# Optimization experiments

Measured on AMD Instinct MI355X. Metric: run time of the kernel, lower is better.

The kernel has to match this reference:

```python
import jax, jax.numpy as jnp
import numpy as np

N = 50000
E = 800000
P = 400000
D_IN = 128
D_HID = 128


def setup_inputs() -> dict:
    key = jax.random.key(0)
    k = jax.random.split(key, 7)
    edge_index = jax.random.randint(k[0], (2, E), 0, N, dtype=jnp.int32)
    edge_pairs = jax.random.randint(k[1], (2, P), 0, N, dtype=jnp.int32)
    emb = jax.random.normal(k[2], (N, D_IN), dtype=jnp.float32)
    W1 = jax.random.normal(k[3], (D_IN, D_HID), dtype=jnp.float32) * (1.0 / np.sqrt(D_IN))
    b1 = jnp.zeros((D_HID,), dtype=jnp.float32)
    W2 = jax.random.normal(k[4], (D_HID, D_HID), dtype=jnp.float32) * (1.0 / np.sqrt(D_HID))
    b2 = jnp.zeros((D_HID,), dtype=jnp.float32)
    return {"edge_index": edge_index, "edge_pairs": edge_pairs, "emb": emb,
            "W1": W1, "b1": b1, "W2": W2, "b2": b2}


def gcn_conv(x, W, b, src, dst):
    """PyG GCNConv: add self-loops, symmetric deg^-1/2 normalization,
    linear transform, scatter-add aggregation into destination nodes."""
    n = x.shape[0]
    loop = jnp.arange(n, dtype=src.dtype)
    s = jnp.concatenate([src, loop])  # [E+N]
    d = jnp.concatenate([dst, loop])
    deg = jax.ops.segment_sum(jnp.ones_like(d, dtype=x.dtype), d, num_segments=n)
    dinv = jnp.where(deg > 0, jax.lax.rsqrt(jnp.maximum(deg, 1e-12)), 0.0)
    norm = dinv[s] * dinv[d]  # [E+N]
    h = x @ W  # [N, out]
    msg = h[s] * norm[:, None]  # gather + scale
    out = jax.ops.segment_sum(msg, d, num_segments=n)  # scatter-add
    return out + b


def reference(edge_index, edge_pairs, emb, W1, b1, W2, b2):
    src, dst = edge_index[0], edge_index[1]
    # encode (eval mode: dropout is identity)
    z = jax.nn.relu(gcn_conv(emb, W1, b1, src, dst))
    z = gcn_conv(z, W2, b2, src, dst)
    # decode: dot product per candidate pair
    return jnp.sum(z[edge_pairs[0]] * z[edge_pairs[1]], axis=1)  # [P]
```

## Files before the change

kernel.cpp:

```cpp
#include <hip/hip_runtime.h>


typedef __attribute__((ext_vector_type(8))) short short8;
typedef __attribute__((ext_vector_type(4))) float floatx4;

#define STAGE_G 128

__device__ __forceinline__ unsigned short f2bf(float f) {
    union { float f; unsigned int u; } v; v.f = f;
    unsigned int u = v.u;
    u += 0x7fffu + ((u >> 16) & 1u);
    return (unsigned short)(u >> 16);
}

__device__ __forceinline__ unsigned int pack2(float a, float b) {
    return (unsigned int)f2bf(a) | ((unsigned int)f2bf(b) << 16);
}

__device__ __forceinline__ float4 cvt4(unsigned int lo, unsigned int hi) {
    float4 f;
    f.x = __uint_as_float(lo << 16);
    f.y = __uint_as_float(lo & 0xffff0000u);
    f.z = __uint_as_float(hi << 16);
    f.w = __uint_as_float(hi & 0xffff0000u);
    return f;
}


__global__ __launch_bounds__(256) void block_hist_kernel(const int* __restrict__ dst,
                                                         int* __restrict__ bhist,
                                                         int E, int NB) {
    __shared__ int bh[1024];
    int t = threadIdx.x, g = blockIdx.x;
    for (int b = t; b < NB; b += 256) bh[b] = 0;
    __syncthreads();
    int chunk = (E + gridDim.x - 1) / gridDim.x;
    int lo = g * chunk, hi = min(lo + chunk, E);
    for (int i = lo + t; i < hi; i += 256) atomicAdd(&bh[dst[i] >> 6], 1);
    __syncthreads();
    for (int b = t; b < NB; b += 256) bhist[g * NB + b] = bh[b];
}

__global__ __launch_bounds__(128) void s1_scan_blocks(int* __restrict__ bhist,
                                                      int* __restrict__ T, int NB) {
    __shared__ int s[2][128];
    int b = blockIdx.x, t = threadIdx.x;
    int v = bhist[t * NB + b];
    int cur = 0;
    s[0][t] = v;
    __syncthreads();
#pragma unroll
    for (int off = 1; off < 128; off <<= 1) {
        int nxt = cur ^ 1;
        int val = s[cur][t];
        if (t >= off) val += s[cur][t - off];
        s[nxt][t] = val;
        __syncthreads();
        cur = nxt;
    }
    int inc = s[cur][t];
    bhist[t * NB + b] = inc - v;
    if (t == 127) T[b] = inc;
}

__global__ __launch_bounds__(256) void s2_scan_buckets(const int* __restrict__ T,
                                                       int* __restrict__ bucket_base, int NB) {
    __shared__ int sums[256];
    int t = threadIdx.x;
    int chunk = (NB + 255) >> 8;
    int lo = t * chunk, hi = min(lo + chunk, NB);
    int s = 0;
    for (int i = lo; i < hi; ++i) s += T[i];
    sums[t] = s;
    __syncthreads();
    if (t == 0) {
        int run = 0;
        for (int i = 0; i < 256; ++i) { int v = sums[i]; sums[i] = run; run += v; }
    }
    __syncthreads();
    int run = sums[t];
    for (int i = lo; i < hi; ++i) { bucket_base[i] = run; run += T[i]; }
    if (lo < NB && hi == NB) bucket_base[NB] = run;
}

__global__ __launch_bounds__(256) void stage_kernel(const int* __restrict__ src,
                                                    const int* __restrict__ dst,
                                                    const int* __restrict__ bhist,
                                                    const int* __restrict__ bucket_base,
                                                    unsigned int* __restrict__ stage,
                                                    int E, int NB) {
    __shared__ int lcur[1024];
    int t = threadIdx.x, g = blockIdx.x;
    for (int b = t; b < NB; b += 256) lcur[b] = bucket_base[b] + bhist[g * NB + b];
    __syncthreads();
    int chunk = (E + gridDim.x - 1) / gridDim.x;
    int lo = g * chunk, hi = min(lo + chunk, E);
    for (int i = lo + t; i < hi; i += 256) {
        int d = dst[i];
        int pos = atomicAdd(&lcur[d >> 6], 1);
        stage[pos] = ((unsigned int)src[i] << 6) | (unsigned int)(d & 63);
    }
}

__global__ __launch_bounds__(256) void scatter_kernel(const unsigned int* __restrict__ stage,
                                                      const int* __restrict__ bucket_base,
                                                      int* __restrict__ row_ptr,
                                                      float* __restrict__ dinv,
                                                      int* __restrict__ srcs_sorted,
                                                      int N) {
    __shared__ int cnt[64];
    __shared__ int lcur[64];
    int b = blockIdx.x, t = threadIdx.x;
    int lo = b << 6;
    int base = bucket_base[b], basen = bucket_base[b + 1];
    if (t < 64) cnt[t] = 0;
    __syncthreads();
    for (int i = base + t; i < basen; i += 256) atomicAdd(&cnt[stage[i] & 63u], 1);
    __syncthreads();
    if (t < 64) {
        int v = cnt[t];
        int inc = v;
#pragma unroll
        for (int off = 1; off < 64; off <<= 1) {
            int x = __shfl_up(inc, off, 64);
            if (t >= off) inc += x;
        }
        int exc = inc - v;
        int node = lo + t;
        if (node < N) {
            row_ptr[node] = base + exc;
            dinv[node] = rsqrtf((float)(v + 1));
            if (node == N - 1) row_ptr[N] = base + exc + v;
        }
        lcur[t] = base + exc;
    }
    __syncthreads();
    for (int i = base + t; i < basen; i += 256) {
        unsigned int rec = stage[i];
        int pos = atomicAdd(&lcur[rec & 63u], 1);
        srcs_sorted[pos] = (int)(rec >> 6);
    }
}

template <bool BF16IN>
__global__ __launch_bounds__(256) void gemm_mfma_kernel(const void* __restrict__ Xv,
                                                        const float* __restrict__ W,
                                                        const float* __restrict__ dinv,
                                                        uint2* __restrict__ H, int N) {
    __shared__ __align__(16) char smem[50176];
    short* WB = (short*)smem;
    short* XL = (short*)(smem + 32768);
    float* Cst = (float*)smem;

    const int tid = threadIdx.x;
    const int w = tid >> 6;
    const int lane = tid & 63;
    const int blk = blockIdx.x;

    {
        const float4* W4 = (const float4*)W;
#pragma unroll
        for (int i = 0; i < 16; ++i) {
            int f = tid + i * 256;
            int k = f >> 5;
            int c4 = f & 31;
            float4 wv = W4[f];
            int kt = k >> 5, q = (k >> 3) & 3, j = k & 7;
            float e[4] = {wv.x, wv.y, wv.z, wv.w};
#pragma unroll
            for (int m = 0; m < 4; ++m) {
                int c = c4 * 4 + m;
                int nt = c >> 4;
                int ln = q * 16 + (c & 15);
                WB[((nt * 4 + kt) * 64 + ln) * 8 + j] = (short)f2bf(e[m]);
            }
        }
    }
    {
#pragma unroll
        for (int i = 0; i < 8; ++i) {
            int f = tid + i * 256;
            int row = f >> 5;
            int c4 = f & 31;
            int gr = min(blk * 64 + row, N - 1);
            uint2 u;
            if constexpr (BF16IN) {
                u = ((const uint2*)Xv)[(size_t)gr * 32 + c4];
            } else {
                float4 xv = ((const float4*)Xv)[(size_t)gr * 32 + c4];
                u.x = pack2(xv.x, xv.y);
                u.y = pack2(xv.z, xv.w);
            }
            *(uint2*)&XL[row * 136 + c4 * 4] = u;
        }
    }
    __syncthreads();

    const int arow = w * 16 + (lane & 15);
    const int koff = (lane >> 4) * 8;
    short8 a[4];
#pragma unroll
    for (int kt = 0; kt < 4; ++kt)
        a[kt] = *(const short8*)&XL[arow * 136 + kt * 32 + koff];

    floatx4 acc[8];
#pragma unroll
    for (int nt = 0; nt < 8; ++nt) acc[nt] = (floatx4){0.f, 0.f, 0.f, 0.f};

#pragma unroll
    for (int kt = 0; kt < 4; ++kt) {
#pragma unroll
        for (int nt = 0; nt < 8; ++nt) {
            short8 b = *(const short8*)&WB[((nt * 4 + kt) * 64 + lane) * 8];
            acc[nt] = __builtin_amdgcn_mfma_f32_16x16x32_bf16(a[kt], b, acc[nt], 0, 0, 0);
        }
    }
    __syncthreads();

    {
        int q = lane >> 4, cn = lane & 15;
#pragma unroll
        for (int nt = 0; nt < 8; ++nt)
#pragma unroll
            for (int r = 0; r < 4; ++r)
                Cst[(w * 16 + q * 4 + r) * 132 + nt * 16 + cn] = acc[nt][r];
    }
    __syncthreads();
    {
#pragma unroll
        for (int i = 0; i < 8; ++i) {
            int f = tid + i * 256;
            int row = f >> 5;
            int c4 = f & 31;
            int gr = blk * 64 + row;
            if (gr < N) {
                float4 v = *(float4*)&Cst[row * 132 + c4 * 4];
                float di = dinv[gr];
                uint2 o;
                o.x = pack2(v.x * di, v.y * di);
                o.y = pack2(v.z * di, v.w * di);
                H[(size_t)gr * 32 + c4] = o;
            }
        }
    }
}

__global__ __launch_bounds__(256) void agg_kernel(const unsigned short* __restrict__ Hp,
                                                  const int* __restrict__ row_ptr,
                                                  const int* __restrict__ srcs,
                                                  const float* __restrict__ dinv,
                                                  const float* __restrict__ bias,
                                                  unsigned short* __restrict__ Z,
                                                  int N, int do_relu) {
    int gw = (int)((blockIdx.x * blockDim.x + threadIdx.x) >> 6);
    int lane = threadIdx.x & 63;
    int q = lane >> 4;
    int hl = lane & 15;
    int n = gw * 4 + q;
    if (n >= N) return;

    const uint4* H4 = (const uint4*)Hp;
    uint4 us = H4[(size_t)n * 16 + hl];
    float4 a0 = cvt4(us.x, us.y);
    float4 a1 = cvt4(us.z, us.w);
    float4 b0 = make_float4(0.f, 0.f, 0.f, 0.f);
    float4 b1 = make_float4(0.f, 0.f, 0.f, 0.f);

    int j = row_ptr[n], end = row_ptr[n + 1];
    for (; j + 7 < end; j += 8) {
        uint4 u0 = H4[(size_t)srcs[j + 0] * 16 + hl];
        uint4 u1 = H4[(size_t)srcs[j + 1] * 16 + hl];
        uint4 u2 = H4[(size_t)srcs[j + 2] * 16 + hl];
        uint4 u3 = H4[(size_t)srcs[j + 3] * 16 + hl];
        uint4 u4 = H4[(size_t)srcs[j + 4] * 16 + hl];
        uint4 u5 = H4[(size_t)srcs[j + 5] * 16 + hl];
        uint4 u6 = H4[(size_t)srcs[j + 6] * 16 + hl];
        uint4 u7 = H4[(size_t)srcs[j + 7] * 16 + hl];
        float4 t;
        t = cvt4(u0.x, u0.y); a0.x += t.x; a0.y += t.y; a0.z += t.z; a0.w += t.w;
        t = cvt4(u0.z, u0.w); a1.x += t.x; a1.y += t.y; a1.z += t.z; a1.w += t.w;
        t = cvt4(u1.x, u1.y); b0.x += t.x; b0.y += t.y; b0.z += t.z; b0.w += t.w;
        t = cvt4(u1.z, u1.w); b1.x += t.x; b1.y += t.y; b1.z += t.z; b1.w += t.w;
        t = cvt4(u2.x, u2.y); a0.x += t.x; a0.y += t.y; a0.z += t.z; a0.w += t.w;
        t = cvt4(u2.z, u2.w); a1.x += t.x; a1.y += t.y; a1.z += t.z; a1.w += t.w;
        t = cvt4(u3.x, u3.y); b0.x += t.x; b0.y += t.y; b0.z += t.z; b0.w += t.w;
        t = cvt4(u3.z, u3.w); b1.x += t.x; b1.y += t.y; b1.z += t.z; b1.w += t.w;
        t = cvt4(u4.x, u4.y); a0.x += t.x; a0.y += t.y; a0.z += t.z; a0.w += t.w;
        t = cvt4(u4.z, u4.w); a1.x += t.x; a1.y += t.y; a1.z += t.z; a1.w += t.w;
        t = cvt4(u5.x, u5.y); b0.x += t.x; b0.y += t.y; b0.z += t.z; b0.w += t.w;
        t = cvt4(u5.z, u5.w); b1.x += t.x; b1.y += t.y; b1.z += t.z; b1.w += t.w;
        t = cvt4(u6.x, u6.y); a0.x += t.x; a0.y += t.y; a0.z += t.z; a0.w += t.w;
        t = cvt4(u6.z, u6.w); a1.x += t.x; a1.y += t.y; a1.z += t.z; a1.w += t.w;
        t = cvt4(u7.x, u7.y); b0.x += t.x; b0.y += t.y; b0.z += t.z; b0.w += t.w;
        t = cvt4(u7.z, u7.w); b1.x += t.x; b1.y += t.y; b1.z += t.z; b1.w += t.w;
    }
    for (; j + 3 < end; j += 4) {
        uint4 u0 = H4[(size_t)srcs[j + 0] * 16 + hl];
        uint4 u1 = H4[(size_t)srcs[j + 1] * 16 + hl];
        uint4 u2 = H4[(size_t)srcs[j + 2] * 16 + hl];
        uint4 u3 = H4[(size_t)srcs[j + 3] * 16 + hl];
        float4 t;
        t = cvt4(u0.x, u0.y); a0.x += t.x; a0.y += t.y; a0.z += t.z; a0.w += t.w;
        t = cvt4(u0.z, u0.w); a1.x += t.x; a1.y += t.y; a1.z += t.z; a1.w += t.w;
        t = cvt4(u1.x, u1.y); b0.x += t.x; b0.y += t.y; b0.z += t.z; b0.w += t.w;
        t = cvt4(u1.z, u1.w); b1.x += t.x; b1.y += t.y; b1.z += t.z; b1.w += t.w;
        t = cvt4(u2.x, u2.y); a0.x += t.x; a0.y += t.y; a0.z += t.z; a0.w += t.w;
        t = cvt4(u2.z, u2.w); a1.x += t.x; a1.y += t.y; a1.z += t.z; a1.w += t.w;
        t = cvt4(u3.x, u3.y); b0.x += t.x; b0.y += t.y; b0.z += t.z; b0.w += t.w;
        t = cvt4(u3.z, u3.w); b1.x += t.x; b1.y += t.y; b1.z += t.z; b1.w += t.w;
    }
    for (; j < end; ++j) {
        uint4 u = H4[(size_t)srcs[j] * 16 + hl];
        float4 t;
        t = cvt4(u.x, u.y); a0.x += t.x; a0.y += t.y; a0.z += t.z; a0.w += t.w;
        t = cvt4(u.z, u.w); a1.x += t.x; a1.y += t.y; a1.z += t.z; a1.w += t.w;
    }
    a0.x += b0.x; a0.y += b0.y; a0.z += b0.z; a0.w += b0.w;
    a1.x += b1.x; a1.y += b1.y; a1.z += b1.z; a1.w += b1.w;

    float di = dinv[n];
    float4 bv0 = ((const float4*)bias)[2 * hl];
    float4 bv1 = ((const float4*)bias)[2 * hl + 1];
    float o0 = di * a0.x + bv0.x, o1 = di * a0.y + bv0.y;
    float o2 = di * a0.z + bv0.z, o3 = di * a0.w + bv0.w;
    float o4 = di * a1.x + bv1.x, o5 = di * a1.y + bv1.y;
    float o6 = di * a1.z + bv1.z, o7 = di * a1.w + bv1.w;
    if (do_relu) {
        o0 = fmaxf(o0, 0.f); o1 = fmaxf(o1, 0.f); o2 = fmaxf(o2, 0.f); o3 = fmaxf(o3, 0.f);
        o4 = fmaxf(o4, 0.f); o5 = fmaxf(o5, 0.f); o6 = fmaxf(o6, 0.f); o7 = fmaxf(o7, 0.f);
    }
    uint4 o;
    o.x = pack2(o0, o1);
    o.y = pack2(o2, o3);
    o.z = pack2(o4, o5);
    o.w = pack2(o6, o7);
    ((uint4*)Z)[(size_t)n * 16 + hl] = o;
}

__global__ __launch_bounds__(256) void decode_kernel(const unsigned short* __restrict__ Z,
                                                     const int* __restrict__ pa,
                                                     const int* __restrict__ pb,
                                                     float* __restrict__ out, int P) {
    int wv = (int)((blockIdx.x * blockDim.x + threadIdx.x) >> 6);
    int lane = threadIdx.x & 63;
    int q = lane >> 4;
    int hl = lane & 15;
    int p0 = wv * 8 + q * 2;
    if (p0 >= P) return;
    const uint4* Z4 = (const uint4*)Z;

    bool two = (p0 + 1 < P);
    int A0 = pa[p0], B0 = pb[p0];
    int A1 = two ? pa[p0 + 1] : A0;
    int B1 = two ? pb[p0 + 1] : B0;
    uint4 ua0 = Z4[(size_t)A0 * 16 + hl];
    uint4 ub0 = Z4[(size_t)B0 * 16 + hl];
    uint4 ua1 = Z4[(size_t)A1 * 16 + hl];
    uint4 ub1 = Z4[(size_t)B1 * 16 + hl];

    float4 xa, xb, ya, yb;
    xa = cvt4(ua0.x, ua0.y); xb = cvt4(ub0.x, ub0.y);
    ya = cvt4(ua0.z, ua0.w); yb = cvt4(ub0.z, ub0.w);
    float v0 = xa.x * xb.x + xa.y * xb.y + xa.z * xb.z + xa.w * xb.w
             + ya.x * yb.x + ya.y * yb.y + ya.z * yb.z + ya.w * yb.w;
    xa = cvt4(ua1.x, ua1.y); xb = cvt4(ub1.x, ub1.y);
    ya = cvt4(ua1.z, ua1.w); yb = cvt4(ub1.z, ub1.w);
    float v1 = xa.x * xb.x + xa.y * xb.y + xa.z * xb.z + xa.w * xb.w
             + ya.x * yb.x + ya.y * yb.y + ya.z * yb.z + ya.w * yb.w;
#pragma unroll
    for (int off = 8; off > 0; off >>= 1) {
        v0 += __shfl_down(v0, off, 16);
        v1 += __shfl_down(v1, off, 16);
    }
    if (hl == 0) {
        out[p0] = v0;
        if (two) out[p0 + 1] = v1;
    }
}

extern "C" void kernel_launch(void* const* d_in, const int* in_sizes, int n_in,
                              void* d_out, int out_size, void* d_ws, size_t ws_size,
                              hipStream_t stream) {
    const int*   edge_index = (const int*)d_in[0];
    const int*   edge_pairs = (const int*)d_in[1];
    const float* emb        = (const float*)d_in[2];
    const float* W1         = (const float*)d_in[3];
    const float* b1         = (const float*)d_in[4];
    const float* W2         = (const float*)d_in[5];
    const float* b2         = (const float*)d_in[6];
    float* out = (float*)d_out;

    int E = in_sizes[0] / 2;
    int P = in_sizes[1] / 2;
    int N = in_sizes[2] / 128;
    int NB = (N + 63) / 64;

    const int* src = edge_index;
    const int* dst = edge_index + E;
    const int* pa  = edge_pairs;
    const int* pb  = edge_pairs + P;

    char* ws = (char*)d_ws;
    size_t off = 0;
    auto alloc = [&](size_t bytes) -> void* {
        void* p = ws + off;
        off = (off + bytes + 255) & ~(size_t)255;
        return p;
    };
    unsigned short* bufA = (unsigned short*)alloc((size_t)N * 128 * 2);
    unsigned short* bufB = (unsigned short*)alloc((size_t)N * 128 * 2);
    int*   srcs_sorted  = (int*)alloc((size_t)E * sizeof(int));
    unsigned int* stage = (unsigned int*)alloc((size_t)E * sizeof(unsigned int));
    int*   row_ptr      = (int*)alloc((size_t)(N + 1) * sizeof(int));
    float* dinv         = (float*)alloc((size_t)N * sizeof(float));
    int*   bhist        = (int*)alloc((size_t)STAGE_G * NB * sizeof(int));
    int*   T            = (int*)alloc((size_t)NB * sizeof(int));
    int*   bucket_base  = (int*)alloc((size_t)(NB + 1) * sizeof(int));

    block_hist_kernel<<<STAGE_G, 256, 0, stream>>>(dst, bhist, E, NB);
    s1_scan_blocks<<<NB, 128, 0, stream>>>(bhist, T, NB);
    s2_scan_buckets<<<1, 256, 0, stream>>>(T, bucket_base, NB);
    stage_kernel<<<STAGE_G, 256, 0, stream>>>(src, dst, bhist, bucket_base, stage, E, NB);
    scatter_kernel<<<NB, 256, 0, stream>>>(stage, bucket_base, row_ptr, dinv, srcs_sorted, N);

    gemm_mfma_kernel<false><<<(N + 63) / 64, 256, 0, stream>>>(emb, W1, dinv, (uint2*)bufA, N);
    agg_kernel<<<(N + 15) / 16, 256, 0, stream>>>(bufA, row_ptr, srcs_sorted, dinv, b1, bufB, N, 1);

    gemm_mfma_kernel<true><<<(N + 63) / 64, 256, 0, stream>>>(bufB, W2, dinv, (uint2*)bufA, N);
    agg_kernel<<<(N + 15) / 16, 256, 0, stream>>>(bufA, row_ptr, srcs_sorted, dinv, b2, bufB, N, 0);

    decode_kernel<<<(P + 31) / 32, 256, 0, stream>>>(bufB, pa, pb, out, P);
}
```

Baseline: 251.1 us.

## Fuse layer-1 aggregation with layer-2 GEMM and fold bucket scan into staging

The layer-1 neighbor aggregation (with bias and ReLU) is now done inside a new kernel that writes the aggregated rows straight into shared memory as the GEMM A tile and then runs the W2 MFMA GEMM. This removes one launch and the round trip of the intermediate Z through global memory. Separately, the single-block bucket scan kernel is dropped and each stage_kernel block recomputes the prefix over T itself, with block 0 writing bucket_base. The cost is redundant scan work in every staging block, and aggregation parallelism of 64 nodes per block with 16 lanes per node, which may give less latency hiding than the old agg kernel's layout.

```diff
diff --git a/kernel.cpp b/kernel.cpp
--- a/kernel.cpp
+++ b/kernel.cpp
@@ -63,36 +63,50 @@
     if (t == 127) T[b] = inc;
 }
 
-__global__ __launch_bounds__(256) void s2_scan_buckets(const int* __restrict__ T,
-                                                       int* __restrict__ bucket_base, int NB) {
-    __shared__ int sums[256];
-    int t = threadIdx.x;
-    int chunk = (NB + 255) >> 8;
-    int lo = t * chunk, hi = min(lo + chunk, NB);
-    int s = 0;
-    for (int i = lo; i < hi; ++i) s += T[i];
-    sums[t] = s;
-    __syncthreads();
-    if (t == 0) {
-        int run = 0;
-        for (int i = 0; i < 256; ++i) { int v = sums[i]; sums[i] = run; run += v; }
-    }
-    __syncthreads();
-    int run = sums[t];
-    for (int i = lo; i < hi; ++i) { bucket_base[i] = run; run += T[i]; }
-    if (lo < NB && hi == NB) bucket_base[NB] = run;
-}
-
 __global__ __launch_bounds__(256) void stage_kernel(const int* __restrict__ src,
                                                     const int* __restrict__ dst,
                                                     const int* __restrict__ bhist,
-                                                    const int* __restrict__ bucket_base,
+                                                    const int* __restrict__ T,
+                                                    int* __restrict__ bucket_base,
                                                     unsigned int* __restrict__ stage,
                                                     int E, int NB) {
     __shared__ int lcur[1024];
+    __shared__ int sb[2][256];
     int t = threadIdx.x, g = blockIdx.x;
-    for (int b = t; b < NB; b += 256) lcur[b] = bucket_base[b] + bhist[g * NB + b];
-    __syncthreads();
+
+    int b0 = t * 4;
+    int v[4];
+    int s = 0;
+#pragma unroll
+    for (int i = 0; i < 4; ++i) {
+        int b = b0 + i;
+        v[i] = (b < NB) ? T[b] : 0;
+        s += v[i];
+    }
+    int cur = 0;
+    sb[0][t] = s;
+    __syncthreads();
+#pragma unroll
+    for (int off = 1; off < 256; off <<= 1) {
+        int val = sb[cur][t];
+        if (t >= off) val += sb[cur][t - off];
+        sb[cur ^ 1][t] = val;
+        __syncthreads();
+        cur ^= 1;
+    }
+    int run = sb[cur][t] - s;
+#pragma unroll
+    for (int i = 0; i < 4; ++i) {
+        int b = b0 + i;
+        if (b < NB) {
+            lcur[b] = run + bhist[(size_t)g * NB + b];
+            if (g == 0) bucket_base[b] = run;
+        }
+        run += v[i];
+    }
+    if (g == 0 && t == 255) bucket_base[NB] = run;
+    __syncthreads();
+
     int chunk = (E + gridDim.x - 1) / gridDim.x;
     int lo = g * chunk, hi = min(lo + chunk, E);
     for (int i = lo + t; i < hi; i += 256) {
@@ -142,8 +156,7 @@
     }
 }
 
-template <bool BF16IN>
-__global__ __launch_bounds__(256) void gemm_mfma_kernel(const void* __restrict__ Xv,
+__global__ __launch_bounds__(256) void gemm_mfma_kernel(const float* __restrict__ Xv,
                                                         const float* __restrict__ W,
                                                         const float* __restrict__ dinv,
                                                         uint2* __restrict__ H, int N) {
@@ -183,14 +196,10 @@
             int row = f >> 5;
             int c4 = f & 31;
             int gr = min(blk * 64 + row, N - 1);
+            float4 xv = ((const float4*)Xv)[(size_t)gr * 32 + c4];
             uint2 u;
-            if constexpr (BF16IN) {
-                u = ((const uint2*)Xv)[(size_t)gr * 32 + c4];
-            } else {
-                float4 xv = ((const float4*)Xv)[(size_t)gr * 32 + c4];
-                u.x = pack2(xv.x, xv.y);
-                u.y = pack2(xv.z, xv.w);
-            }
+            u.x = pack2(xv.x, xv.y);
+            u.y = pack2(xv.z, xv.w);
             *(uint2*)&XL[row * 136 + c4 * 4] = u;
         }
     }
@@ -240,6 +249,154 @@
                 o.x = pack2(v.x * di, v.y * di);
                 o.y = pack2(v.z * di, v.w * di);
                 H[(size_t)gr * 32 + c4] = o;
+            }
+        }
+    }
+}
+
+__global__ __launch_bounds__(256) void agg_gemm_kernel(const unsigned short* __restrict__ Hp,
+                                                       const int* __restrict__ row_ptr,
+                                                       const int* __restrict__ srcs,
+                                                       const float* __restrict__ dinv,
+                                                       const float* __restrict__ bias1,
+                                                       const float* __restrict__ W2,
+                                                       uint2* __restrict__ Hout, int N) {
+    __shared__ __align__(16) char smem[50176];
+    short* WB = (short*)smem;
+    short* XL = (short*)(smem + 32768);
+    float* Cst = (float*)smem;
+
+    const int tid = threadIdx.x;
+    const int blk = blockIdx.x;
+
+    {
+        const float4* W4 = (const float4*)W2;
+#pragma unroll
+        for (int i = 0; i < 16; ++i) {
+            int f = tid + i * 256;
+            int k = f >> 5;
+            int c4 = f & 31;
+            float4 wv = W4[f];
+            int kt = k >> 5, q = (k >> 3) & 3, j = k & 7;
+            float e[4] = {wv.x, wv.y, wv.z, wv.w};
+#pragma unroll
+            for (int m = 0; m < 4; ++m) {
+                int c = c4 * 4 + m;
+                int nt = c >> 4;
+                int ln = q * 16 + (c & 15);
+                WB[((nt * 4 + kt) * 64 + ln) * 8 + j] = (short)f2bf(e[m]);
+            }
+        }
+    }
+
+    {
+        int qw = tid >> 4;
+        int hl = tid & 15;
+        const uint4* H4 = (const uint4*)Hp;
+        float4 bv0 = ((const float4*)bias1)[2 * hl];
+        float4 bv1 = ((const float4*)bias1)[2 * hl + 1];
+#pragma unroll
+        for (int r = 0; r < 4; ++r) {
+            int idx = qw + 16 * r;
+            int n = blk * 64 + idx;
+            uint4 o;
+            if (n < N) {
+                uint4 us = H4[(size_t)n * 16 + hl];
+                float4 a0 = cvt4(us.x, us.y);
+                float4 a1 = cvt4(us.z, us.w);
+                float4 c0 = make_float4(0.f, 0.f, 0.f, 0.f);
+                float4 c1 = make_float4(0.f, 0.f, 0.f, 0.f);
+                int j = row_ptr[n], end = row_ptr[n + 1];
+                for (; j + 3 < end; j += 4) {
+                    uint4 u0 = H4[(size_t)srcs[j + 0] * 16 + hl];
+                    uint4 u1 = H4[(size_t)srcs[j + 1] * 16 + hl];
+                    uint4 u2 = H4[(size_t)srcs[j + 2] * 16 + hl];
+                    uint4 u3 = H4[(size_t)srcs[j + 3] * 16 + hl];
+                    float4 t;
+                    t = cvt4(u0.x, u0.y); a0.x += t.x; a0.y += t.y; a0.z += t.z; a0.w += t.w;
+                    t = cvt4(u0.z, u0.w); a1.x += t.x; a1.y += t.y; a1.z += t.z; a1.w += t.w;
+                    t = cvt4(u1.x, u1.y); c0.x += t.x; c0.y += t.y; c0.z += t.z; c0.w += t.w;
+                    t = cvt4(u1.z, u1.w); c1.x += t.x; c1.y += t.y; c1.z += t.z; c1.w += t.w;
+                    t = cvt4(u2.x, u2.y); a0.x += t.x; a0.y += t.y; a0.z += t.z; a0.w += t.w;
+                    t = cvt4(u2.z, u2.w); a1.x += t.x; a1.y += t.y; a1.z += t.z; a1.w += t.w;
+                    t = cvt4(u3.x, u3.y); c0.x += t.x; c0.y += t.y; c0.z += t.z; c0.w += t.w;
+                    t = cvt4(u3.z, u3.w); c1.x += t.x; c1.y += t.y; c1.z += t.z; c1.w += t.w;
+                }
+                for (; j < end; ++j) {
+                    uint4 u = H4[(size_t)srcs[j] * 16 + hl];
+                    float4 t;
+                    t = cvt4(u.x, u.y); a0.x += t.x; a0.y += t.y; a0.z += t.z; a0.w += t.w;
+                    t = cvt4(u.z, u.w); a1.x += t.x; a1.y += t.y; a1.z += t.z; a1.w += t.w;
+                }
+                a0.x += c0.x; a0.y += c0.y; a0.z += c0.z; a0.w += c0.w;
+                a1.x += c1.x; a1.y += c1.y; a1.z += c1.z; a1.w += c1.w;
+                float di = dinv[n];
+                float o0 = fmaxf(di * a0.x + bv0.x, 0.f);
+                float o1 = fmaxf(di * a0.y + bv0.y, 0.f);
+                float o2 = fmaxf(di * a0.z + bv0.z, 0.f);
+                float o3 = fmaxf(di * a0.w + bv0.w, 0.f);
+                float o4 = fmaxf(di * a1.x + bv1.x, 0.f);
+                float o5 = fmaxf(di * a1.y + bv1.y, 0.f);
+                float o6 = fmaxf(di * a1.z + bv1.z, 0.f);
+                float o7 = fmaxf(di * a1.w + bv1.w, 0.f);
+                o.x = pack2(o0, o1);
+                o.y = pack2(o2, o3);
+                o.z = pack2(o4, o5);
+                o.w = pack2(o6, o7);
+            } else {
+                o = make_uint4(0u, 0u, 0u, 0u);
+            }
+            *(uint4*)&XL[idx * 136 + hl * 8] = o;
+        }
+    }
+    __syncthreads();
+
+    const int w = tid >> 6;
+    const int lane = tid & 63;
+    const int arow = w * 16 + (lane & 15);
+    const int koff = (lane >> 4) * 8;
+    short8 a[4];
+#pragma unroll
+    for (int kt = 0; kt < 4; ++kt)
+        a[kt] = *(const short8*)&XL[arow * 136 + kt * 32 + koff];
+
+    floatx4 acc[8];
+#pragma unroll
+    for (int nt = 0; nt < 8; ++nt) acc[nt] = (floatx4){0.f, 0.f, 0.f, 0.f};
+
+#pragma unroll
+    for (int kt = 0; kt < 4; ++kt) {
+#pragma unroll
+        for (int nt = 0; nt < 8; ++nt) {
+            short8 b = *(const short8*)&WB[((nt * 4 + kt) * 64 + lane) * 8];
+            acc[nt] = __builtin_amdgcn_mfma_f32_16x16x32_bf16(a[kt], b, acc[nt], 0, 0, 0);
+        }
+    }
+    __syncthreads();
+
+    {
+        int q = lane >> 4, cn = lane & 15;
+#pragma unroll
+        for (int nt = 0; nt < 8; ++nt)
+#pragma unroll
+            for (int r = 0; r < 4; ++r)
+                Cst[(w * 16 + q * 4 + r) * 132 + nt * 16 + cn] = acc[nt][r];
+    }
+    __syncthreads();
+    {
+#pragma unroll
+        for (int i = 0; i < 8; ++i) {
+            int f = tid + i * 256;
+            int row = f >> 5;
+            int c4 = f & 31;
+            int gr = blk * 64 + row;
+            if (gr < N) {
+                float4 v = *(float4*)&Cst[row * 132 + c4 * 4];
+                float di = dinv[gr];
+                uint2 o;
+                o.x = pack2(v.x * di, v.y * di);
+                o.y = pack2(v.z * di, v.w * di);
+                Hout[(size_t)gr * 32 + c4] = o;
             }
         }
     }
@@ -419,15 +576,16 @@
 
     block_hist_kernel<<<STAGE_G, 256, 0, stream>>>(dst, bhist, E, NB);
     s1_scan_blocks<<<NB, 128, 0, stream>>>(bhist, T, NB);
-    s2_scan_buckets<<<1, 256, 0, stream>>>(T, bucket_base, NB);
-    stage_kernel<<<STAGE_G, 256, 0, stream>>>(src, dst, bhist, bucket_base, stage, E, NB);
+    stage_kernel<<<STAGE_G, 256, 0, stream>>>(src, dst, bhist, T, bucket_base, stage, E, NB);
     scatter_kernel<<<NB, 256, 0, stream>>>(stage, bucket_base, row_ptr, dinv, srcs_sorted, N);
 
-    gemm_mfma_kernel<false><<<(N + 63) / 64, 256, 0, stream>>>(emb, W1, dinv, (uint2*)bufA, N);
-    agg_kernel<<<(N + 15) / 16, 256, 0, stream>>>(bufA, row_ptr, srcs_sorted, dinv, b1, bufB, N, 1);
-
-    gemm_mfma_kernel<true><<<(N + 63) / 64, 256, 0, stream>>>(bufB, W2, dinv, (uint2*)bufA, N);
-    agg_kernel<<<(N + 15) / 16, 256, 0, stream>>>(bufA, row_ptr, srcs_sorted, dinv, b2, bufB, N, 0);
-
-    decode_kernel<<<(P + 31) / 32, 256, 0, stream>>>(bufB, pa, pb, out, P);
-}
+    gemm_mfma_kernel<<<(N + 63) / 64, 256, 0, stream>>>(emb, W1, dinv, (uint2*)bufA, N);
+
+    agg_gemm_kernel<<<(N + 63) / 64, 256, 0, stream>>>(bufA, row_ptr, srcs_sorted, dinv,
+                                                       b1, W2, (uint2*)bufB, N);
+
+    agg_kernel<<<(N + 15) / 16, 256, 0, stream>>>(bufB, row_ptr, srcs_sorted, dinv, b2,
+                                                  (unsigned short*)bufA, N, 0);
+
+    decode_kernel<<<(P + 31) / 32, 256, 0, stream>>>((unsigned short*)bufA, pa, pb, out, P);
+}
```

New measurement: 260.3 us. 3.7% more time.
